# Kernel optimization log

Hardware: AMD Instinct MI355X
Metric: run time of the kernel (lower is better)

## Reference

```python
import jax, jax.numpy as jnp
import numpy as np

B, S, D = 1, 2048, 2048
H, KVH, HD = 16, 8, 128
ROPE_THETA = 1e6
P_POW, C_SHIFT = 8, 7.0
MASK_VAL = -7.0  # = -c so masked bpmax base ~ scores only (finite under ^8)


def rotate_half(x):
    x1, x2 = jnp.split(x, 2, axis=-1)
    return jnp.concatenate([-x2, x1], axis=-1)


def setup_inputs() -> dict:
    key = jax.random.key(0)
    ks = jax.random.split(key, 10)
    hidden_states = jax.random.normal(ks[0], (B, S, D), dtype=jnp.float32)
    # RoPE tables (Qwen3-style, theta=1e6)
    inv_freq = 1.0 / (ROPE_THETA ** (jnp.arange(0, HD, 2, dtype=jnp.float32) / HD))
    freqs = jnp.arange(S, dtype=jnp.float32)[:, None] * inv_freq[None, :]
    emb = jnp.concatenate([freqs, freqs], axis=-1)  # [S, HD]
    cos = jnp.broadcast_to(jnp.cos(emb)[None], (B, S, HD)).astype(jnp.float32)
    sin = jnp.broadcast_to(jnp.sin(emb)[None], (B, S, HD)).astype(jnp.float32)
    sc = D ** -0.5
    q_proj_w = jax.random.normal(ks[1], (D, H * HD), dtype=jnp.float32) * sc
    k_proj_w = jax.random.normal(ks[2], (D, KVH * HD), dtype=jnp.float32) * sc
    v_proj_w = jax.random.normal(ks[3], (D, KVH * HD), dtype=jnp.float32) * sc
    o_proj_w = jax.random.normal(ks[4], (H * HD, D), dtype=jnp.float32) * (H * HD) ** -0.5
    q_norm_w = jnp.ones((HD,), dtype=jnp.float32)
    k_norm_w = jnp.ones((HD,), dtype=jnp.float32)
    # Stored RMSNorm denominators (rsqrt-like buffers from training), ~O(1)
    q_denom = 0.5 + jax.random.uniform(ks[5], (B, S, H, 1), dtype=jnp.float32)
    k_denom = 0.5 + jax.random.uniform(ks[6], (B, S, KVH, 1), dtype=jnp.float32)
    # Stored bpmax normalizer buffer rd (per-head, per-query-row)
    rd = 5.0 + 10.0 * jax.random.uniform(ks[7], (1, H, S, 1), dtype=jnp.float32)
    # Causal mask with MASK_VAL for masked positions (finite under bpmax)
    causal = jnp.tril(jnp.ones((S, S), dtype=bool))
    attention_mask = jnp.where(causal, 0.0, MASK_VAL)[None, None].astype(jnp.float32)
    return {
        'hidden_states': hidden_states, 'cos': cos, 'sin': sin,
        'q_proj_w': q_proj_w, 'k_proj_w': k_proj_w, 'v_proj_w': v_proj_w,
        'o_proj_w': o_proj_w, 'q_norm_w': q_norm_w, 'k_norm_w': k_norm_w,
        'q_denom': q_denom, 'k_denom': k_denom, 'rd': rd,
        'attention_mask': attention_mask,
    }


def reference(hidden_states, cos, sin, q_proj_w, k_proj_w, v_proj_w, o_proj_w,
              q_norm_w, k_norm_w, q_denom, k_denom, rd, attention_mask):
    b, s, d = hidden_states.shape
    hd = q_norm_w.shape[0]
    scaling = hd ** -0.5
    # Projections + per-head RMSNorm (eval path: stored denominator buffer)
    q = (hidden_states @ q_proj_w).reshape(b, s, -1, hd)
    q = (q_norm_w * (q * q_denom[:, :s])).transpose(0, 2, 1, 3)   # [B,H,S,hd]
    k = (hidden_states @ k_proj_w).reshape(b, s, -1, hd)
    k = (k_norm_w * (k * k_denom[:, :s])).transpose(0, 2, 1, 3)   # [B,KVH,S,hd]
    v = (hidden_states @ v_proj_w).reshape(b, s, -1, hd).transpose(0, 2, 1, 3)
    # RoPE
    cos_ = cos[:, None, :, :]
    sin_ = sin[:, None, :, :]
    q = q * cos_ + rotate_half(q) * sin_
    k = k * cos_ + rotate_half(k) * sin_
    # GQA: repeat kv heads
    groups = q.shape[1] // k.shape[1]
    k = jnp.repeat(k, groups, axis=1)
    v = jnp.repeat(v, groups, axis=1)
    # Scores + mask + bpmax power-law normalization (eval path)
    aw = jnp.einsum('bhqd,bhkd->bhqk', q, k) * scaling
    aw = aw + attention_mask[:, :, :, :s]
    aw = ((aw + C_SHIFT) / rd[:, :, :s, :]) ** P_POW
    # Attention output + output projection
    out = jnp.einsum('bhqk,bhkd->bhqd', aw, v)
    out = out.transpose(0, 2, 1, 3).reshape(b, s, -1)
    return out @ o_proj_w
```

## Files before the change

### kernel.cpp

```cpp
#include <hip/hip_runtime.h>
#include <cstdint>
#include <cstddef>


namespace {
constexpr int kS = 2048;
constexpr int kD = 2048;
constexpr int kH = 16;
constexpr int kKVH = 8;
constexpr int kHD = 128;
constexpr float kScale = 0.08838834764831845f;
constexpr size_t MB = 1u << 20;
}

using f32x4 = __attribute__((ext_vector_type(4))) float;
using bfrag = __attribute__((ext_vector_type(8))) short;
using float4v = __attribute__((ext_vector_type(4))) float;
using short4v = __attribute__((ext_vector_type(4))) short;

__device__ __forceinline__ unsigned short f2b(float f) {
  union { float f; unsigned u; } x; x.f = f;
  unsigned r = x.u + 0x7FFFu + ((x.u >> 16) & 1u);
  return (unsigned short)(r >> 16);
}

__device__ __forceinline__ void gload_lds16(const void* g, void* l) {
  __builtin_amdgcn_global_load_lds(
      (const __attribute__((address_space(1))) unsigned*)g,
      (__attribute__((address_space(3))) unsigned*)l, 16, 0, 0);
}

__global__ __launch_bounds__(256) void qwen_cast_bf16(const float* __restrict__ in,
                                                      unsigned short* __restrict__ out,
                                                      int n4) {
  int i = blockIdx.x * 256 + threadIdx.x;
  if (i >= n4) return;
  float4v v = *(const float4v*)(in + (size_t)i * 4);
  short4v o;
  o[0] = (short)f2b(v[0]); o[1] = (short)f2b(v[1]);
  o[2] = (short)f2b(v[2]); o[3] = (short)f2b(v[3]);
  *(short4v*)(out + (size_t)i * 4) = o;
}

__global__ __launch_bounds__(256) void qwen_tw(const float* __restrict__ in, int R, int C,
                                               unsigned short* __restrict__ out, int ldo) {
  __shared__ float t[64][65];
  int c0 = blockIdx.x * 64, r0 = blockIdx.y * 64;
  int tr = threadIdx.x >> 6, tc = threadIdx.x & 63;
#pragma unroll
  for (int p = 0; p < 16; ++p) {
    int i = p * 4 + tr;
    t[i][tc] = in[(size_t)(r0 + i) * C + c0 + tc];
  }
  __syncthreads();
#pragma unroll
  for (int p = 0; p < 16; ++p) {
    int i = p * 4 + tr;
    out[(size_t)(c0 + i) * ldo + r0 + tc] = f2b(t[tc][i]);
  }
}

template <int BM>
__global__ __launch_bounds__(256) void qwen_gemm_bt(const unsigned short* __restrict__ A,
                                                    const unsigned short* __restrict__ Bt,
                                                    float* __restrict__ C,
                                                    int M, int N, int K) {
  __shared__ unsigned short As[2][BM * 32];
  __shared__ unsigned short Bs[2][128 * 32];
  constexpr int MR = BM / 32;
  const int nwg = gridDim.x * gridDim.y;
  int lin = blockIdx.y * gridDim.x + blockIdx.x;
  if ((nwg & 7) == 0) { int qq = nwg >> 3; lin = (lin & 7) * qq + (lin >> 3); }
  const int bxx = lin % gridDim.x, byy = lin / gridDim.x;
  const int tid = threadIdx.x, lane = tid & 63, w = tid >> 6;
  const int wr = w >> 1, wc = w & 1;
  const int row0 = bxx * BM, col0 = byy * 128;
  f32x4 acc[MR][4] = {};
  const int koff = (lane >> 4) << 3;
  const int rA = wr * (BM / 2) + (lane & 15);
  const int rB = wc * 64 + (lane & 15);

  auto stage = [&](int kt, int b) {
#pragma unroll
    for (int c = 0; c < BM / 64; ++c) {
      int off = (c * 256 + tid) * 16;
      int e = off >> 1;
      int r = e >> 5, cc = e & 31;
      gload_lds16(A + (size_t)(row0 + r) * K + kt + cc, (char*)(&As[b][0]) + off);
    }
#pragma unroll
    for (int c = 0; c < 2; ++c) {
      int off = (c * 256 + tid) * 16;
      int e = off >> 1;
      int r = e >> 5, cc = e & 31;
      gload_lds16(Bt + (size_t)(col0 + r) * K + kt + cc, (char*)(&Bs[b][0]) + off);
    }
  };

  const int nk = K >> 5;
  stage(0, 0);
  asm volatile("s_waitcnt vmcnt(0)" ::: "memory");
  __builtin_amdgcn_s_barrier();
  int buf = 0;
#pragma unroll 1
  for (int t = 0; t < nk; ++t) {
    if (t + 1 < nk) stage((t + 1) << 5, buf ^ 1);
    bfrag aF[MR], bF[4];
#pragma unroll
    for (int m = 0; m < MR; ++m)
      aF[m] = *(const bfrag*)(&As[buf][0] + (rA + m * 16) * 32 + koff);
#pragma unroll
    for (int n = 0; n < 4; ++n)
      bF[n] = *(const bfrag*)(&Bs[buf][0] + (rB + n * 16) * 32 + koff);
#pragma unroll
    for (int m = 0; m < MR; ++m)
#pragma unroll
      for (int n = 0; n < 4; ++n)
        acc[m][n] = __builtin_amdgcn_mfma_f32_16x16x32_bf16(aF[m], bF[n], acc[m][n], 0, 0, 0);
    asm volatile("s_waitcnt vmcnt(0)" ::: "memory");
    __builtin_amdgcn_s_barrier();
    buf ^= 1;
  }
  const int cr = (lane >> 4) << 2;
  const int cc2 = lane & 15;
#pragma unroll
  for (int m = 0; m < MR; ++m)
#pragma unroll
    for (int n = 0; n < 4; ++n) {
      int r = row0 + wr * (BM / 2) + m * 16 + cr;
      int c = col0 + wc * 64 + n * 16 + cc2;
#pragma unroll
      for (int j = 0; j < 4; ++j) C[(size_t)(r + j) * N + c] = acc[m][n][j];
    }
}

__global__ __launch_bounds__(256) void qwen_rope_qk(const float* __restrict__ Cqkv,
                                                    const float* __restrict__ cosb,
                                                    const float* __restrict__ sinb,
                                                    const float* __restrict__ qnw,
                                                    const float* __restrict__ knw,
                                                    const float* __restrict__ qden,
                                                    const float* __restrict__ kden,
                                                    unsigned short* __restrict__ Qb,
                                                    unsigned short* __restrict__ Kswz) {
  int s = blockIdx.x;
  int t = threadIdx.x;
  const float* row = Cqkv + (size_t)s * 4096;
  const float* cs = cosb + (size_t)s * kHD;
  const float* sn = sinb + (size_t)s * kHD;
#pragma unroll
  for (int rep = 0; rep < 8; ++rep) {
    int idx = rep * 256 + t;
    int h = idx >> 7, d = idx & 127;
    float dn = qden[s * kH + h];
    float v = row[idx] * dn * qnw[d];
    float pv = row[(h << 7) + (d ^ 64)] * dn * qnw[d ^ 64];
    float rot = (d < 64) ? -pv : pv;
    Qb[((size_t)h * kS + s) * kHD + d] = f2b(v * cs[d] + rot * sn[d]);
  }
  const int kt = s >> 6, key = s & 63;
#pragma unroll
  for (int rep = 0; rep < 4; ++rep) {
    int idx = rep * 256 + t;
    int h = idx >> 7, d = idx & 127;
    float dn = kden[s * kKVH + h];
    float v = row[2048 + idx] * dn * knw[d];
    float pv = row[2048 + (h << 7) + (d ^ 64)] * dn * knw[d ^ 64];
    float rot = (d < 64) ? -pv : pv;
    size_t rowi = ((size_t)(h * 32 + kt) * 64 + key) * 128;
    Kswz[rowi + (d ^ ((key & 7) << 3))] = f2b(v * cs[d] + rot * sn[d]);
  }
}

__global__ __launch_bounds__(256) void qwen_vtr(const float* __restrict__ Cqkv,
                                                unsigned short* __restrict__ Vswz) {
  __shared__ float t[64][65];
  int kvh = blockIdx.x, st = blockIdx.y, dt = blockIdx.z;
  int s0 = st * 64, d0 = dt * 64;
  int tr = threadIdx.x >> 6, tc = threadIdx.x & 63;
#pragma unroll
  for (int p = 0; p < 16; ++p) {
    int i = p * 4 + tr;
    t[i][tc] = Cqkv[(size_t)(s0 + i) * 4096 + 3072 + (kvh << 7) + d0 + tc];
  }
  __syncthreads();
#pragma unroll
  for (int p = 0; p < 16; ++p) {
    int i = p * 4 + tr;
    int d = d0 + i;
    size_t rowi = ((size_t)(kvh * 32 + st) * 128 + d) * 64;
    Vswz[rowi + (tc ^ ((d & 7) << 2))] = f2b(t[tc][i]);
  }
}

#define STAGE8(cc, bb)                                                 \
  do {                                                                 \
    const char* ks_ = Ksrc + ((size_t)(cc) << 14) + tid * 16;          \
    const char* vs_ = Vsrc + ((size_t)(cc) << 14) + tid * 16;          \
    char* kd_ = (char*)(&KV[bb][0]) + tid * 16;                        \
    char* vd_ = (char*)(&KV[2 + (bb)][0]) + tid * 16;                  \
    _Pragma("unroll") for (int it = 0; it < 4; ++it) {                 \
      gload_lds16(ks_ + it * 4096, kd_ + it * 4096);                   \
      gload_lds16(vs_ + it * 4096, vd_ + it * 4096);                   \
    }                                                                  \
  } while (0)

__global__ __launch_bounds__(256, 2) void qwen_attn(const unsigned short* __restrict__ Qb,
                                                    const unsigned short* __restrict__ Kswz,
                                                    const unsigned short* __restrict__ Vswz,
                                                    const float* __restrict__ rd,
                                                    unsigned short* __restrict__ AO) {
  __shared__ unsigned short KV[4][8192];
  const int bid = blockIdx.x;
  const int kvh = bid & 7;
  const int h = kvh * 2 + ((bid >> 3) & 1);
  const int qt = 31 - (bid >> 4);
  const int q0 = qt * 64;
  const int nch = qt + 1;
  const int tid = threadIdx.x, lane = tid & 63, w = tid >> 6;
  const int l15 = lane & 15, g = lane >> 4;
  const int qw0 = q0 + w * 16;
  const int qlim = qw0 + l15;
  const int swzK = (l15 & 7) << 3;
  const int swzV = (l15 & 7) << 2;

  bfrag qF[4];
#pragma unroll
  for (int dc = 0; dc < 4; ++dc)
    qF[dc] = *(const bfrag*)(Qb + ((size_t)h * kS + qw0 + l15) * kHD + dc * 32 + g * 8);
  const float inv = 1.0f / rd[(size_t)h * kS + qw0 + l15];

  const char* Ksrc = (const char*)Kswz + ((size_t)(kvh * 32) << 14);
  const char* Vsrc = (const char*)Vswz + ((size_t)(kvh * 32) << 14);

  f32x4 outa[8] = {};

  STAGE8(0, 0);
#pragma unroll 1
  for (int c = 0; c < nch; ++c) {
    const int b = c & 1;
    if (c + 1 < nch) {
      STAGE8(c + 1, b ^ 1);
      asm volatile("s_waitcnt vmcnt(8)" ::: "memory");
    } else {
      asm volatile("s_waitcnt vmcnt(0)" ::: "memory");
    }
    __builtin_amdgcn_s_barrier();
    const unsigned short* Kbuf = &KV[b][0];
    const unsigned short* Vbuf = &KV[2 + b][0];
    f32x4 sc[4] = {};
#pragma unroll
    for (int t = 0; t < 4; ++t) {
      const unsigned short* kr = Kbuf + (t * 16 + l15) * 128;
#pragma unroll
      for (int dc = 0; dc < 4; ++dc) {
        bfrag kf = *(const bfrag*)(kr + ((dc * 32 + g * 8) ^ swzK));
        sc[t] = __builtin_amdgcn_mfma_f32_16x16x32_bf16(kf, qF[dc], sc[t], 0, 0, 0);
      }
    }
    const int kbase = c * 64;
    const bool full = (c < qt);
    union { bfrag f; unsigned u[4]; } pb[2];
#pragma unroll
    for (int t = 0; t < 4; ++t) {
      unsigned short bb[4];
#pragma unroll
      for (int rr = 0; rr < 4; ++rr) {
        float tt = sc[t][rr] * kScale;
        int key = kbase + t * 16 + g * 4 + rr;
        tt += (full || key <= qlim) ? 7.0f : 0.0f;
        float y = tt * inv;
        float y2 = y * y, y4 = y2 * y2;
        bb[rr] = f2b(y4 * y4);
      }
      pb[t >> 1].u[(t & 1) * 2 + 0] = (unsigned)bb[0] | ((unsigned)bb[1] << 16);
      pb[t >> 1].u[(t & 1) * 2 + 1] = (unsigned)bb[2] | ((unsigned)bb[3] << 16);
    }
#pragma unroll
    for (int dt = 0; dt < 8; ++dt) {
      const unsigned short* vr = Vbuf + (dt * 16 + l15) * 64;
#pragma unroll
      for (int pr = 0; pr < 2; ++pr) {
        union { bfrag f; short4v h4[2]; } va;
        va.h4[0] = *(const short4v*)(vr + ((pr * 32 + g * 4) ^ swzV));
        va.h4[1] = *(const short4v*)(vr + ((pr * 32 + 16 + g * 4) ^ swzV));
        outa[dt] = __builtin_amdgcn_mfma_f32_16x16x32_bf16(va.f, pb[pr].f, outa[dt], 0, 0, 0);
      }
    }
    __builtin_amdgcn_s_barrier();
  }
#pragma unroll
  for (int dt = 0; dt < 8; ++dt) {
    short4v o;
    o[0] = (short)f2b(outa[dt][0]); o[1] = (short)f2b(outa[dt][1]);
    o[2] = (short)f2b(outa[dt][2]); o[3] = (short)f2b(outa[dt][3]);
    *(short4v*)(AO + (size_t)(qw0 + l15) * kD + h * 128 + dt * 16 + g * 4) = o;
  }
}

extern "C" void kernel_launch(void* const* d_in, const int* in_sizes, int n_in,
                              void* d_out, int out_size, void* d_ws, size_t ws_size,
                              hipStream_t stream) {
  (void)in_sizes; (void)n_in; (void)out_size; (void)ws_size;
  const float* hidden = (const float*)d_in[0];
  const float* cosb   = (const float*)d_in[1];
  const float* sinb   = (const float*)d_in[2];
  const float* qw     = (const float*)d_in[3];
  const float* kw     = (const float*)d_in[4];
  const float* vw     = (const float*)d_in[5];
  const float* ow     = (const float*)d_in[6];
  const float* qnw    = (const float*)d_in[7];
  const float* knw    = (const float*)d_in[8];
  const float* qden   = (const float*)d_in[9];
  const float* kden   = (const float*)d_in[10];
  const float* rd     = (const float*)d_in[11];
  float* out = (float*)d_out;

  char* ws = (char*)d_ws;
  unsigned short* hsb  = (unsigned short*)(ws + 0 * MB);
  unsigned short* Wt   = (unsigned short*)(ws + 8 * MB);
  float*          Cqkv = (float*)(ws + 24 * MB);
  unsigned short* Qb   = (unsigned short*)(ws + 56 * MB);
  unsigned short* Kswz = (unsigned short*)(ws + 64 * MB);
  unsigned short* Vswz = (unsigned short*)(ws + 68 * MB);
  unsigned short* AO   = (unsigned short*)(ws + 72 * MB);
  unsigned short* Ot   = (unsigned short*)(ws + 80 * MB);

  qwen_cast_bf16<<<4096, 256, 0, stream>>>(hidden, hsb, 2048 * 2048 / 4);
  qwen_tw<<<dim3(32, 32), 256, 0, stream>>>(qw, 2048, 2048, Wt, 2048);
  qwen_tw<<<dim3(16, 32), 256, 0, stream>>>(kw, 2048, 1024, Wt + (size_t)2048 * 2048, 2048);
  qwen_tw<<<dim3(16, 32), 256, 0, stream>>>(vw, 2048, 1024, Wt + (size_t)3072 * 2048, 2048);
  qwen_tw<<<dim3(32, 32), 256, 0, stream>>>(ow, 2048, 2048, Ot, 2048);
  qwen_gemm_bt<128><<<dim3(16, 32), 256, 0, stream>>>(hsb, Wt, Cqkv, 2048, 4096, 2048);
  qwen_rope_qk<<<2048, 256, 0, stream>>>(Cqkv, cosb, sinb, qnw, knw, qden, kden, Qb, Kswz);
  qwen_vtr<<<dim3(8, 32, 2), 256, 0, stream>>>(Cqkv, Vswz);
  qwen_attn<<<512, 256, 0, stream>>>(Qb, Kswz, Vswz, rd, AO);
  qwen_gemm_bt<128><<<dim3(16, 16), 256, 0, stream>>>(AO, Ot, out, 2048, 2048, 2048);
}
```

Baseline: 180.7 us.

## Process 128 query rows per attention block to reuse staged K/V tiles

Each attention block now covers 128 query rows instead of 64, with every wave holding two 16-row Q fragment sets. Each K/V chunk staged in LDS therefore feeds twice as many MFMAs, which halves total K/V global traffic and the number of staging barriers per query row. The grid shrinks from 512 to 256 blocks, so per-CU occupancy and latency hiding drop, and the register footprint grows. The V swizzle is widened to 16 rows, changed in both the transpose writer and the attention reader, presumably to reduce LDS bank conflicts.

```diff
diff --git a/kernel.cpp b/kernel.cpp
--- a/kernel.cpp
+++ b/kernel.cpp
@@ -189,7 +189,7 @@
     int i = p * 4 + tr;
     int d = d0 + i;
     size_t rowi = ((size_t)(kvh * 32 + st) * 128 + d) * 64;
-    Vswz[rowi + (tc ^ ((d & 7) << 2))] = f2b(t[tc][i]);
+    Vswz[rowi + (tc ^ ((d & 15) << 2))] = f2b(t[tc][i]);
   }
 }
 
@@ -214,26 +214,31 @@
   const int bid = blockIdx.x;
   const int kvh = bid & 7;
   const int h = kvh * 2 + ((bid >> 3) & 1);
-  const int qt = 31 - (bid >> 4);
-  const int q0 = qt * 64;
-  const int nch = qt + 1;
+  const int qt = 15 - (bid >> 4);
+  const int q0 = qt * 128;
+  const int nch = 2 * qt + 2;
   const int tid = threadIdx.x, lane = tid & 63, w = tid >> 6;
   const int l15 = lane & 15, g = lane >> 4;
-  const int qw0 = q0 + w * 16;
-  const int qlim = qw0 + l15;
+  const int qw0 = q0 + w * 32;
+  const int qlim0 = qw0 + l15;
+  const int qlim1 = qw0 + 16 + l15;
   const int swzK = (l15 & 7) << 3;
-  const int swzV = (l15 & 7) << 2;
-
-  bfrag qF[4];
-#pragma unroll
-  for (int dc = 0; dc < 4; ++dc)
-    qF[dc] = *(const bfrag*)(Qb + ((size_t)h * kS + qw0 + l15) * kHD + dc * 32 + g * 8);
-  const float inv = 1.0f / rd[(size_t)h * kS + qw0 + l15];
+  const int swzV = l15 << 2;
+
+  bfrag qF[2][4];
+#pragma unroll
+  for (int qs = 0; qs < 2; ++qs)
+#pragma unroll
+    for (int dc = 0; dc < 4; ++dc)
+      qF[qs][dc] = *(const bfrag*)(Qb + ((size_t)h * kS + qw0 + qs * 16 + l15) * kHD +
+                                   dc * 32 + g * 8);
+  const float inv[2] = {1.0f / rd[(size_t)h * kS + qlim0],
+                        1.0f / rd[(size_t)h * kS + qlim1]};
 
   const char* Ksrc = (const char*)Kswz + ((size_t)(kvh * 32) << 14);
   const char* Vsrc = (const char*)Vswz + ((size_t)(kvh * 32) << 14);
 
-  f32x4 outa[8] = {};
+  f32x4 outa[2][8] = {};
 
   STAGE8(0, 0);
 #pragma unroll 1
@@ -248,33 +253,39 @@
     __builtin_amdgcn_s_barrier();
     const unsigned short* Kbuf = &KV[b][0];
     const unsigned short* Vbuf = &KV[2 + b][0];
-    f32x4 sc[4] = {};
+    f32x4 sc[2][4] = {};
 #pragma unroll
     for (int t = 0; t < 4; ++t) {
       const unsigned short* kr = Kbuf + (t * 16 + l15) * 128;
 #pragma unroll
       for (int dc = 0; dc < 4; ++dc) {
         bfrag kf = *(const bfrag*)(kr + ((dc * 32 + g * 8) ^ swzK));
-        sc[t] = __builtin_amdgcn_mfma_f32_16x16x32_bf16(kf, qF[dc], sc[t], 0, 0, 0);
+        sc[0][t] = __builtin_amdgcn_mfma_f32_16x16x32_bf16(kf, qF[0][dc], sc[0][t], 0, 0, 0);
+        sc[1][t] = __builtin_amdgcn_mfma_f32_16x16x32_bf16(kf, qF[1][dc], sc[1][t], 0, 0, 0);
       }
     }
     const int kbase = c * 64;
-    const bool full = (c < qt);
-    union { bfrag f; unsigned u[4]; } pb[2];
-#pragma unroll
-    for (int t = 0; t < 4; ++t) {
-      unsigned short bb[4];
-#pragma unroll
-      for (int rr = 0; rr < 4; ++rr) {
-        float tt = sc[t][rr] * kScale;
-        int key = kbase + t * 16 + g * 4 + rr;
-        tt += (full || key <= qlim) ? 7.0f : 0.0f;
-        float y = tt * inv;
-        float y2 = y * y, y4 = y2 * y2;
-        bb[rr] = f2b(y4 * y4);
+    const bool full = (kbase + 63 <= qw0);
+    union { bfrag f; unsigned u[4]; } pb[2][2];
+#pragma unroll
+    for (int qs = 0; qs < 2; ++qs) {
+      const int ql = qs ? qlim1 : qlim0;
+      const float iv = inv[qs];
+#pragma unroll
+      for (int t = 0; t < 4; ++t) {
+        unsigned short bb[4];
+#pragma unroll
+        for (int rr = 0; rr < 4; ++rr) {
+          float tt = sc[qs][t][rr] * kScale;
+          int key = kbase + t * 16 + g * 4 + rr;
+          tt += (full || key <= ql) ? 7.0f : 0.0f;
+          float y = tt * iv;
+          float y2 = y * y, y4 = y2 * y2;
+          bb[rr] = f2b(y4 * y4);
+        }
+        pb[qs][t >> 1].u[(t & 1) * 2 + 0] = (unsigned)bb[0] | ((unsigned)bb[1] << 16);
+        pb[qs][t >> 1].u[(t & 1) * 2 + 1] = (unsigned)bb[2] | ((unsigned)bb[3] << 16);
       }
-      pb[t >> 1].u[(t & 1) * 2 + 0] = (unsigned)bb[0] | ((unsigned)bb[1] << 16);
-      pb[t >> 1].u[(t & 1) * 2 + 1] = (unsigned)bb[2] | ((unsigned)bb[3] << 16);
     }
 #pragma unroll
     for (int dt = 0; dt < 8; ++dt) {
@@ -284,18 +295,21 @@
         union { bfrag f; short4v h4[2]; } va;
         va.h4[0] = *(const short4v*)(vr + ((pr * 32 + g * 4) ^ swzV));
         va.h4[1] = *(const short4v*)(vr + ((pr * 32 + 16 + g * 4) ^ swzV));
-        outa[dt] = __builtin_amdgcn_mfma_f32_16x16x32_bf16(va.f, pb[pr].f, outa[dt], 0, 0, 0);
+        outa[0][dt] = __builtin_amdgcn_mfma_f32_16x16x32_bf16(va.f, pb[0][pr].f, outa[0][dt], 0, 0, 0);
+        outa[1][dt] = __builtin_amdgcn_mfma_f32_16x16x32_bf16(va.f, pb[1][pr].f, outa[1][dt], 0, 0, 0);
       }
     }
     __builtin_amdgcn_s_barrier();
   }
 #pragma unroll
-  for (int dt = 0; dt < 8; ++dt) {
-    short4v o;
-    o[0] = (short)f2b(outa[dt][0]); o[1] = (short)f2b(outa[dt][1]);
-    o[2] = (short)f2b(outa[dt][2]); o[3] = (short)f2b(outa[dt][3]);
-    *(short4v*)(AO + (size_t)(qw0 + l15) * kD + h * 128 + dt * 16 + g * 4) = o;
-  }
+  for (int qs = 0; qs < 2; ++qs)
+#pragma unroll
+    for (int dt = 0; dt < 8; ++dt) {
+      short4v o;
+      o[0] = (short)f2b(outa[qs][dt][0]); o[1] = (short)f2b(outa[qs][dt][1]);
+      o[2] = (short)f2b(outa[qs][dt][2]); o[3] = (short)f2b(outa[qs][dt][3]);
+      *(short4v*)(AO + (size_t)(qw0 + qs * 16 + l15) * kD + h * 128 + dt * 16 + g * 4) = o;
+    }
 }
 
 extern "C" void kernel_launch(void* const* d_in, const int* in_sizes, int n_in,
@@ -334,6 +348,6 @@
   qwen_gemm_bt<128><<<dim3(16, 32), 256, 0, stream>>>(hsb, Wt, Cqkv, 2048, 4096, 2048);
   qwen_rope_qk<<<2048, 256, 0, stream>>>(Cqkv, cosb, sinb, qnw, knw, qden, kden, Qb, Kswz);
   qwen_vtr<<<dim3(8, 32, 2), 256, 0, stream>>>(Cqkv, Vswz);
-  qwen_attn<<<512, 256, 0, stream>>>(Qb, Kswz, Vswz, rd, AO);
+  qwen_attn<<<256, 256, 0, stream>>>(Qb, Kswz, Vswz, rd, AO);
   qwen_gemm_bt<128><<<dim3(16, 16), 256, 0, stream>>>(AO, Ot, out, 2048, 2048, 2048);
 }
```

Measured after the change: 184.5 us. 1.02x slower.
